# Kernel tuning notes

Hardware: AMD Instinct MI355X
Metric: run time of the kernel (lower is better)

The kernel has to match this reference:

```python
import jax, jax.numpy as jnp
import numpy as np

B, T, L = 512, 512, 128  # batch, seq_len, tag-vocab size (incl. START=126, STOP=127)


def setup_inputs() -> dict:
    key = jax.random.key(0)
    k1, k2, k3 = jax.random.split(key, 3)
    # scale emissions so exp(gold path score) stays finite in fp32
    feats = jax.random.normal(k1, (B, T, L), dtype=jnp.float32) * 0.05
    # xavier_normal on [L, L] -> std = sqrt(2/(L+L)) = 1/sqrt(L)
    transfer = jax.random.normal(k2, (L, L), dtype=jnp.float32) * (1.0 / np.sqrt(L))
    target = jax.random.randint(k3, (B, T), 0, L - 2, dtype=jnp.int32)
    return {"feats": feats, "transfer": transfer, "target": target,
            "start": L - 2, "stop": L - 1}


def _crf_loss(feats, transfer, target, start, stop):
    # feats: [B, T, L] emissions; transfer: [L, L]; target: [B, T] gold tags
    Bb, Tt, Ll = feats.shape

    # ---- forward algorithm (log-sum-exp DP over tags) ----
    # scores[1] = feats[1] + transfer[start, :]
    prev0 = feats[:, 1] + transfer[start][None, :]  # [B, L]

    def step(prev, f_t):
        # original: scores[t, y] = LSE_x( scores[t-1, x] + feats[t, x] + transfer[x, y] )
        v = prev + f_t                                        # [B, L] over prev-tag x
        new = jax.nn.logsumexp(v[:, :, None] + transfer[None, :, :], axis=1)  # [B, L]
        return new, None

    step = jax.checkpoint(step)  # keep scan residuals to just the carries
    feats_rest = jnp.swapaxes(feats[:, 2:], 0, 1)  # [T-2, B, L]
    prev, _ = jax.lax.scan(step, prev0, feats_rest)
    sentence_score = jax.nn.logsumexp(prev + transfer[:, stop][None, :], axis=1)  # [B]

    # ---- gold path score ----
    emit0 = feats[:, 0, start]  # hh[0, start]
    emit = jnp.take_along_axis(feats[:, 1:], target[:, 1:, None], axis=2)[..., 0].sum(axis=1)
    pre = jnp.concatenate(
        [jnp.full((Bb, 1), start, dtype=target.dtype), target[:, 1:Tt - 1]], axis=1)  # [B, T-1]
    # original reads transfer[pre, tgt].data[0] -> detached constant
    trans = jax.lax.stop_gradient(transfer[pre, target[:, 1:]]).sum(axis=1)
    gold_score = jnp.exp(emit0 + emit + trans)  # original returns torch.exp(score)

    return sentence_score - gold_score  # per-sentence loss, shape [B]


def reference(feats, transfer, target, start, stop):
    return _crf_loss(feats, transfer, target, start, stop)
```

## Files before the change

kernel.cpp:

```cpp
#include <hip/hip_runtime.h>

#define T_DIM 512
#define L_DIM 128

typedef _Float16 h2 __attribute__((ext_vector_type(2)));
typedef float f2 __attribute__((ext_vector_type(2)));

#if defined(__has_builtin)
#if __has_builtin(__builtin_amdgcn_fdot2)
#define HAS_FDOT2 1
#endif
#endif

__device__ __forceinline__ float fdot2_acc(h2 a, h2 b, float c) {
#ifdef HAS_FDOT2
    return __builtin_amdgcn_fdot2(a, b, c, false);
#else
    return c + (float)a.x * (float)b.x + (float)a.y * (float)b.y;
#endif
}

__device__ __forceinline__ unsigned int pack_u32(float a, float b) {
    return __builtin_bit_cast(unsigned int, __builtin_amdgcn_cvt_pkrtz(a, b));
}

#define H2C(x) __builtin_bit_cast(h2, (x))


#define E_GROUPS(X) X(0) X(1) X(2) X(3) X(4) X(5) X(6) X(7) \
                    X(8) X(9) X(10) X(11) X(12) X(13) X(14) X(15)

__global__ __launch_bounds__(64, 1) void crf_fwd_kernel(
    const float* __restrict__ feats,
    const float* __restrict__ transfer,
    const int* __restrict__ target,
    const int* __restrict__ startp,
    const int* __restrict__ stopp,
    float* __restrict__ out)
{
    __shared__ unsigned int LdsU[2][64] __attribute__((aligned(16)));

    const int lane = threadIdx.x;
    const int j0   = lane << 1;
    const int b    = blockIdx.x;
    const int start = startp[0];
    const int stop  = stopp[0];
    const float* fbase = feats + (size_t)b * T_DIM * L_DIM;
    const float LOG128 = 4.852030263919617f;
    const float SCALE  = 0.0078125f;

#define DECL_E(v) uint4 EA##v, EB##v;
    E_GROUPS(DECL_E)
#undef DECL_E

#define LD2(r) (*reinterpret_cast<const f2*>(&transfer[(r) * L_DIM + j0]))
#define LOAD_E(v) { \
    f2 r0 = LD2(8*(v)+0), r1 = LD2(8*(v)+1), r2 = LD2(8*(v)+2), r3 = LD2(8*(v)+3); \
    f2 r4 = LD2(8*(v)+4), r5 = LD2(8*(v)+5), r6 = LD2(8*(v)+6), r7 = LD2(8*(v)+7); \
    EA##v.x = pack_u32(__expf(r0.x)*SCALE, __expf(r1.x)*SCALE); \
    EA##v.y = pack_u32(__expf(r2.x)*SCALE, __expf(r3.x)*SCALE); \
    EA##v.z = pack_u32(__expf(r4.x)*SCALE, __expf(r5.x)*SCALE); \
    EA##v.w = pack_u32(__expf(r6.x)*SCALE, __expf(r7.x)*SCALE); \
    EB##v.x = pack_u32(__expf(r0.y)*SCALE, __expf(r1.y)*SCALE); \
    EB##v.y = pack_u32(__expf(r2.y)*SCALE, __expf(r3.y)*SCALE); \
    EB##v.z = pack_u32(__expf(r4.y)*SCALE, __expf(r5.y)*SCALE); \
    EB##v.w = pack_u32(__expf(r6.y)*SCALE, __expf(r7.y)*SCALE); }
    E_GROUPS(LOAD_E)
#undef LOAD_E
#undef LD2

    const float trStop0 = transfer[j0 * L_DIM + stop];
    const float trStop1 = transfer[(j0 + 1) * L_DIM + stop];

    {
        f2 f1v = *reinterpret_cast<const f2*>(&fbase[1 * L_DIM + j0]);
        f2 f2v = *reinterpret_cast<const f2*>(&fbase[2 * L_DIM + j0]);
        f2 tsv = *reinterpret_cast<const f2*>(&transfer[start * L_DIM + j0]);
        LdsU[0][lane] = pack_u32(__expf(f1v.x + f2v.x + tsv.x),
                                 __expf(f1v.y + f2v.y + tsv.y));
    }
    f2 fa2 = *reinterpret_cast<const f2*>(&fbase[3 * L_DIM + j0]);
    f2 fb2 = *reinterpret_cast<const f2*>(&fbase[4 * L_DIM + j0]);
    f2 fc2 = *reinterpret_cast<const f2*>(&fbase[5 * L_DIM + j0]);
    float S = 0.f;
    asm volatile("s_waitcnt lgkmcnt(0)" ::: "memory");

    int cur = 0;
    float accF0 = 0.f, accF1 = 0.f;

    for (int t = 2; t <= T_DIM - 1; ++t) {
        int tp = t + 4; if (tp > T_DIM - 1) tp = T_DIM - 1;
        f2 fnew2 = *reinterpret_cast<const f2*>(&fbase[tp * L_DIM + j0]);
        float e0 = __expf(fa2.x);
        float e1 = __expf(fa2.y);

        if ((t & 15) == 0) {
            h2 h = H2C(LdsU[cur][0]);
            float u0 = (float)h.x;
            float r = 1.0f / u0;
            e0 *= r; e1 *= r;
            S += __logf(u0);
        }

        const uint4* U4p = reinterpret_cast<const uint4*>(&LdsU[cur][0]);
        float s0 = 0.f, s1 = 0.f, s2 = 0.f, s3 = 0.f;
        float q0 = 0.f, q1 = 0.f, q2 = 0.f, q3 = 0.f;

#define DOT_G(v, AC, BC) { \
        uint4 p = U4p[v]; \
        AC = fdot2_acc(H2C(p.x), H2C(EA##v.x), AC); \
        AC = fdot2_acc(H2C(p.y), H2C(EA##v.y), AC); \
        AC = fdot2_acc(H2C(p.z), H2C(EA##v.z), AC); \
        AC = fdot2_acc(H2C(p.w), H2C(EA##v.w), AC); \
        BC = fdot2_acc(H2C(p.x), H2C(EB##v.x), BC); \
        BC = fdot2_acc(H2C(p.y), H2C(EB##v.y), BC); \
        BC = fdot2_acc(H2C(p.z), H2C(EB##v.z), BC); \
        BC = fdot2_acc(H2C(p.w), H2C(EB##v.w), BC); }

        DOT_G(0,  s0, q0) DOT_G(1,  s1, q1) DOT_G(2,  s2, q2) DOT_G(3,  s3, q3)
        DOT_G(4,  s0, q0) DOT_G(5,  s1, q1) DOT_G(6,  s2, q2) DOT_G(7,  s3, q3)
        DOT_G(8,  s0, q0) DOT_G(9,  s1, q1) DOT_G(10, s2, q2) DOT_G(11, s3, q3)
        DOT_G(12, s0, q0) DOT_G(13, s1, q1) DOT_G(14, s2, q2) DOT_G(15, s3, q3)
#undef DOT_G

        float acc0 = (s0 + s1) + (s2 + s3);
        float acc1 = (q0 + q1) + (q2 + q3);

        if (t < T_DIM - 1) {
            LdsU[cur ^ 1][lane] = pack_u32(acc0 * e0, acc1 * e1);
            asm volatile("s_waitcnt lgkmcnt(0)" ::: "memory");
            cur ^= 1;
            fa2 = fb2; fb2 = fc2; fc2 = fnew2;
        } else {
            accF0 = acc0; accF1 = acc1;
        }
    }

    S += 510.0f * LOG128;

    float x0 = __logf(accF0) + S + trStop0;
    float x1 = __logf(accF1) + S + trStop1;
    float mx = fmaxf(x0, x1);
#pragma unroll
    for (int d = 1; d < 64; d <<= 1) mx = fmaxf(mx, __shfl_xor(mx, d));
    float ex = __expf(x0 - mx) + __expf(x1 - mx);
#pragma unroll
    for (int d = 1; d < 64; d <<= 1) ex += __shfl_xor(ex, d);
    float sentence = mx + __logf(ex);

    float es = 0.f, ts = 0.f;
    const int* tgt = target + b * T_DIM;
#pragma unroll
    for (int k = 0; k < 8; ++k) {
        int t = 1 + lane + (k << 6);
        if (t < T_DIM) {
            int tg = tgt[t];
            es += fbase[t * L_DIM + tg];
            int pr = (t == 1) ? start : tgt[t - 1];
            ts += transfer[pr * L_DIM + tg];
        }
    }
#pragma unroll
    for (int d = 1; d < 64; d <<= 1) {
        es += __shfl_xor(es, d);
        ts += __shfl_xor(ts, d);
    }
    if (lane == 0) {
        float emit0 = fbase[start];
        out[b] = sentence - __expf(emit0 + es + ts);
    }
}

extern "C" void kernel_launch(void* const* d_in, const int* in_sizes, int n_in,
                              void* d_out, int out_size, void* d_ws, size_t ws_size,
                              hipStream_t stream) {
    const float* feats    = (const float*)d_in[0];
    const float* transfer = (const float*)d_in[1];
    const int*   target   = (const int*)d_in[2];
    const int*   startp   = (const int*)d_in[3];
    const int*   stopp    = (const int*)d_in[4];
    float* outp = (float*)d_out;
    int B = in_sizes[0] / (T_DIM * L_DIM);
    hipLaunchKernelGGL(crf_fwd_kernel, dim3(B), dim3(64), 0, stream,
                       feats, transfer, target, startp, stopp, outp);
}
```

Baseline: 411.3 us.

## Split CRF forward DP across two wavefronts, one output tag per thread

Each block now uses 128 threads (two wavefronts) instead of 64, and each thread owns one output tag instead of two. This halves the per-thread fdot2 work and the register-resident exp(transfer) column per time step. The price is a workgroup barrier (s_barrier) every step to share the fp16 probability vector through LDS, plus a cross-wave final reduction through shared memory. The 510-step serial chain now pays barrier latency each iteration in exchange for shorter per-thread dot products.

```diff
diff --git a/kernel.cpp b/kernel.cpp
--- a/kernel.cpp
+++ b/kernel.cpp
@@ -4,7 +4,6 @@
 #define L_DIM 128
 
 typedef _Float16 h2 __attribute__((ext_vector_type(2)));
-typedef float f2 __attribute__((ext_vector_type(2)));
 
 #if defined(__has_builtin)
 #if __has_builtin(__builtin_amdgcn_fdot2)
@@ -26,11 +25,15 @@
 
 #define H2C(x) __builtin_bit_cast(h2, (x))
 
+__device__ __forceinline__ void lds_barrier() {
+    asm volatile("s_waitcnt lgkmcnt(0)\n\ts_barrier" ::: "memory");
+}
+
 
 #define E_GROUPS(X) X(0) X(1) X(2) X(3) X(4) X(5) X(6) X(7) \
                     X(8) X(9) X(10) X(11) X(12) X(13) X(14) X(15)
 
-__global__ __launch_bounds__(64, 1) void crf_fwd_kernel(
+__global__ __launch_bounds__(128, 1) void crf_fwd_kernel(
     const float* __restrict__ feats,
     const float* __restrict__ transfer,
     const int* __restrict__ target,
@@ -39,9 +42,12 @@
     float* __restrict__ out)
 {
     __shared__ unsigned int LdsU[2][64] __attribute__((aligned(16)));
+    __shared__ float LdsRed[8];
 
-    const int lane = threadIdx.x;
-    const int j0   = lane << 1;
+    const int tid  = threadIdx.x;
+    const int lane = tid & 63;
+    const int wv   = tid >> 6;
+    const int g    = tid;
     const int b    = blockIdx.x;
     const int start = startp[0];
     const int stop  = stopp[0];
@@ -49,110 +55,98 @@
     const float LOG128 = 4.852030263919617f;
     const float SCALE  = 0.0078125f;
 
-#define DECL_E(v) uint4 EA##v, EB##v;
+#define DECL_E(v) uint4 E##v;
     E_GROUPS(DECL_E)
 #undef DECL_E
 
-#define LD2(r) (*reinterpret_cast<const f2*>(&transfer[(r) * L_DIM + j0]))
+#define LDT(r) transfer[(r) * L_DIM + g]
 #define LOAD_E(v) { \
-    f2 r0 = LD2(8*(v)+0), r1 = LD2(8*(v)+1), r2 = LD2(8*(v)+2), r3 = LD2(8*(v)+3); \
-    f2 r4 = LD2(8*(v)+4), r5 = LD2(8*(v)+5), r6 = LD2(8*(v)+6), r7 = LD2(8*(v)+7); \
-    EA##v.x = pack_u32(__expf(r0.x)*SCALE, __expf(r1.x)*SCALE); \
-    EA##v.y = pack_u32(__expf(r2.x)*SCALE, __expf(r3.x)*SCALE); \
-    EA##v.z = pack_u32(__expf(r4.x)*SCALE, __expf(r5.x)*SCALE); \
-    EA##v.w = pack_u32(__expf(r6.x)*SCALE, __expf(r7.x)*SCALE); \
-    EB##v.x = pack_u32(__expf(r0.y)*SCALE, __expf(r1.y)*SCALE); \
-    EB##v.y = pack_u32(__expf(r2.y)*SCALE, __expf(r3.y)*SCALE); \
-    EB##v.z = pack_u32(__expf(r4.y)*SCALE, __expf(r5.y)*SCALE); \
-    EB##v.w = pack_u32(__expf(r6.y)*SCALE, __expf(r7.y)*SCALE); }
+    float e0 = __expf(LDT(8*(v)+0)) * SCALE, e1 = __expf(LDT(8*(v)+1)) * SCALE; \
+    float e2 = __expf(LDT(8*(v)+2)) * SCALE, e3 = __expf(LDT(8*(v)+3)) * SCALE; \
+    float e4 = __expf(LDT(8*(v)+4)) * SCALE, e5 = __expf(LDT(8*(v)+5)) * SCALE; \
+    float e6 = __expf(LDT(8*(v)+6)) * SCALE, e7 = __expf(LDT(8*(v)+7)) * SCALE; \
+    E##v.x = pack_u32(e0, e1); E##v.y = pack_u32(e2, e3); \
+    E##v.z = pack_u32(e4, e5); E##v.w = pack_u32(e6, e7); }
     E_GROUPS(LOAD_E)
 #undef LOAD_E
-#undef LD2
+#undef LDT
 
-    const float trStop0 = transfer[j0 * L_DIM + stop];
-    const float trStop1 = transfer[(j0 + 1) * L_DIM + stop];
+    const float trStop = transfer[g * L_DIM + stop];
 
     {
-        f2 f1v = *reinterpret_cast<const f2*>(&fbase[1 * L_DIM + j0]);
-        f2 f2v = *reinterpret_cast<const f2*>(&fbase[2 * L_DIM + j0]);
-        f2 tsv = *reinterpret_cast<const f2*>(&transfer[start * L_DIM + j0]);
-        LdsU[0][lane] = pack_u32(__expf(f1v.x + f2v.x + tsv.x),
-                                 __expf(f1v.y + f2v.y + tsv.y));
+        float v2 = fbase[1 * L_DIM + g] + fbase[2 * L_DIM + g]
+                 + transfer[start * L_DIM + g];
+        _Float16 h = (_Float16)__expf(v2);
+        reinterpret_cast<unsigned short*>(&LdsU[0][0])[g] =
+            __builtin_bit_cast(unsigned short, h);
     }
-    f2 fa2 = *reinterpret_cast<const f2*>(&fbase[3 * L_DIM + j0]);
-    f2 fb2 = *reinterpret_cast<const f2*>(&fbase[4 * L_DIM + j0]);
-    f2 fc2 = *reinterpret_cast<const f2*>(&fbase[5 * L_DIM + j0]);
-    float S = 0.f;
-    asm volatile("s_waitcnt lgkmcnt(0)" ::: "memory");
+    float fa = fbase[3 * L_DIM + g];
+    float fb = fbase[4 * L_DIM + g];
+    float fc = fbase[5 * L_DIM + g];
+    float S  = 0.f;
+    lds_barrier();
 
     int cur = 0;
-    float accF0 = 0.f, accF1 = 0.f;
+    float accF = 0.f;
 
     for (int t = 2; t <= T_DIM - 1; ++t) {
         int tp = t + 4; if (tp > T_DIM - 1) tp = T_DIM - 1;
-        f2 fnew2 = *reinterpret_cast<const f2*>(&fbase[tp * L_DIM + j0]);
-        float e0 = __expf(fa2.x);
-        float e1 = __expf(fa2.y);
+        float fnew = fbase[tp * L_DIM + g];
+        float e = __expf(fa);
 
         if ((t & 15) == 0) {
             h2 h = H2C(LdsU[cur][0]);
             float u0 = (float)h.x;
-            float r = 1.0f / u0;
-            e0 *= r; e1 *= r;
+            e *= 1.0f / u0;
             S += __logf(u0);
         }
 
         const uint4* U4p = reinterpret_cast<const uint4*>(&LdsU[cur][0]);
         float s0 = 0.f, s1 = 0.f, s2 = 0.f, s3 = 0.f;
-        float q0 = 0.f, q1 = 0.f, q2 = 0.f, q3 = 0.f;
 
-#define DOT_G(v, AC, BC) { \
+#define DOT_G(v, AC) { \
         uint4 p = U4p[v]; \
-        AC = fdot2_acc(H2C(p.x), H2C(EA##v.x), AC); \
-        AC = fdot2_acc(H2C(p.y), H2C(EA##v.y), AC); \
-        AC = fdot2_acc(H2C(p.z), H2C(EA##v.z), AC); \
-        AC = fdot2_acc(H2C(p.w), H2C(EA##v.w), AC); \
-        BC = fdot2_acc(H2C(p.x), H2C(EB##v.x), BC); \
-        BC = fdot2_acc(H2C(p.y), H2C(EB##v.y), BC); \
-        BC = fdot2_acc(H2C(p.z), H2C(EB##v.z), BC); \
-        BC = fdot2_acc(H2C(p.w), H2C(EB##v.w), BC); }
+        AC = fdot2_acc(H2C(p.x), H2C(E##v.x), AC); \
+        AC = fdot2_acc(H2C(p.y), H2C(E##v.y), AC); \
+        AC = fdot2_acc(H2C(p.z), H2C(E##v.z), AC); \
+        AC = fdot2_acc(H2C(p.w), H2C(E##v.w), AC); }
 
-        DOT_G(0,  s0, q0) DOT_G(1,  s1, q1) DOT_G(2,  s2, q2) DOT_G(3,  s3, q3)
-        DOT_G(4,  s0, q0) DOT_G(5,  s1, q1) DOT_G(6,  s2, q2) DOT_G(7,  s3, q3)
-        DOT_G(8,  s0, q0) DOT_G(9,  s1, q1) DOT_G(10, s2, q2) DOT_G(11, s3, q3)
-        DOT_G(12, s0, q0) DOT_G(13, s1, q1) DOT_G(14, s2, q2) DOT_G(15, s3, q3)
+        DOT_G(0,  s0) DOT_G(1,  s1) DOT_G(2,  s2) DOT_G(3,  s3)
+        DOT_G(4,  s0) DOT_G(5,  s1) DOT_G(6,  s2) DOT_G(7,  s3)
+        DOT_G(8,  s0) DOT_G(9,  s1) DOT_G(10, s2) DOT_G(11, s3)
+        DOT_G(12, s0) DOT_G(13, s1) DOT_G(14, s2) DOT_G(15, s3)
 #undef DOT_G
 
-        float acc0 = (s0 + s1) + (s2 + s3);
-        float acc1 = (q0 + q1) + (q2 + q3);
+        float acc = (s0 + s1) + (s2 + s3);
 
         if (t < T_DIM - 1) {
-            LdsU[cur ^ 1][lane] = pack_u32(acc0 * e0, acc1 * e1);
-            asm volatile("s_waitcnt lgkmcnt(0)" ::: "memory");
+            _Float16 h = (_Float16)(acc * e);
+            reinterpret_cast<unsigned short*>(&LdsU[cur ^ 1][0])[g] =
+                __builtin_bit_cast(unsigned short, h);
+            lds_barrier();
             cur ^= 1;
-            fa2 = fb2; fb2 = fc2; fc2 = fnew2;
+            fa = fb; fb = fc; fc = fnew;
         } else {
-            accF0 = acc0; accF1 = acc1;
+            accF = acc;
         }
     }
 
     S += 510.0f * LOG128;
 
-    float x0 = __logf(accF0) + S + trStop0;
-    float x1 = __logf(accF1) + S + trStop1;
-    float mx = fmaxf(x0, x1);
+    float x  = __logf(accF) + S + trStop;
+    float mx = x;
 #pragma unroll
     for (int d = 1; d < 64; d <<= 1) mx = fmaxf(mx, __shfl_xor(mx, d));
-    float ex = __expf(x0 - mx) + __expf(x1 - mx);
+    float ex = __expf(x - mx);
 #pragma unroll
     for (int d = 1; d < 64; d <<= 1) ex += __shfl_xor(ex, d);
-    float sentence = mx + __logf(ex);
+    if (lane == 0) { LdsRed[wv] = mx; LdsRed[2 + wv] = ex; }
 
     float es = 0.f, ts = 0.f;
     const int* tgt = target + b * T_DIM;
 #pragma unroll
-    for (int k = 0; k < 8; ++k) {
-        int t = 1 + lane + (k << 6);
+    for (int k = 0; k < 4; ++k) {
+        int t = 1 + tid + (k << 7);
         if (t < T_DIM) {
             int tg = tgt[t];
             es += fbase[t * L_DIM + tg];
@@ -165,9 +159,18 @@
         es += __shfl_xor(es, d);
         ts += __shfl_xor(ts, d);
     }
-    if (lane == 0) {
+    if (lane == 0) { LdsRed[4 + wv] = es; LdsRed[6 + wv] = ts; }
+    __syncthreads();
+
+    if (tid == 0) {
+        float M  = fmaxf(LdsRed[0], LdsRed[1]);
+        float Ss = LdsRed[2] * __expf(LdsRed[0] - M)
+                 + LdsRed[3] * __expf(LdsRed[1] - M);
+        float sentence = M + __logf(Ss);
+        float em = LdsRed[4] + LdsRed[5];
+        float tn = LdsRed[6] + LdsRed[7];
         float emit0 = fbase[start];
-        out[b] = sentence - __expf(emit0 + es + ts);
+        out[b] = sentence - __expf(emit0 + em + tn);
     }
 }
 
@@ -181,6 +184,6 @@
     const int*   stopp    = (const int*)d_in[4];
     float* outp = (float*)d_out;
     int B = in_sizes[0] / (T_DIM * L_DIM);
-    hipLaunchKernelGGL(crf_fwd_kernel, dim3(B), dim3(64), 0, stream,
+    hipLaunchKernelGGL(crf_fwd_kernel, dim3(B), dim3(128), 0, stream,
                        feats, transfer, target, startp, stopp, outp);
 }
```

After: 425.9 us. 1.04x slower.
